# Optimization experiments

Measured on AMD Instinct MI355X. Metric: run time of the kernel, lower is better.

Reference implementation:

```python
import jax, jax.numpy as jnp
import numpy as np

DROPOUT_RATE = 0.1  # reference runs deterministically (dropout disabled), matching eval-mode math


def setup_inputs() -> dict:
    key = jax.random.key(0)
    k1, k2, k3 = jax.random.split(key, 3)
    BH, S, D = 32, 2048, 64   # batch*heads, seq_len, d_head
    B = 2                      # true batch (mask batch dim)
    q = jax.random.normal(k1, (BH, S, D), dtype=jnp.float32)
    k = jax.random.normal(k2, (BH, S, D), dtype=jnp.float32)
    v = jax.random.normal(k3, (BH, S, D), dtype=jnp.float32)
    mask = jnp.zeros((B, S, S), dtype=jnp.float32)  # additive mask
    return {"q": q, "k": k, "v": v, "mask": mask}


def reference(q, k, v, mask):
    # Scaled dot-product attention with additive mask.
    # q,k,v: [BH, S, D]; mask: [B, S, S], tiled along batch to BH.
    dk = jnp.asarray(k.shape[-1], dtype=jnp.float32)
    scores = jnp.einsum('bqd,bkd->bqk', q, k) / jnp.sqrt(dk)  # [BH, S, S]
    reps = q.shape[0] // mask.shape[0]
    mask_t = jnp.tile(mask, (reps, 1, 1))                     # [BH, S, S]
    attn = jax.nn.softmax(scores + mask_t, axis=-1)
    out = jnp.einsum('bqk,bkd->bqd', attn, v)                 # [BH, S, D]
    # K.dropout omitted: deterministic reference (eval mode / identity)
    return out
```

## Files before the change

kernel.cpp:

```cpp
#include <hip/hip_runtime.h>


constexpr int cBH = 32;
constexpr int cS  = 2048;
constexpr int cD  = 64;
constexpr int cQT = 128;
constexpr int cNT = cS / 64;

typedef __bf16 bf16x8 __attribute__((ext_vector_type(8)));
typedef __bf16 bf16x4 __attribute__((ext_vector_type(4)));
typedef float  f32x4  __attribute__((ext_vector_type(4)));

__device__ __forceinline__ unsigned short bfbits(float f) {
    return __builtin_bit_cast(unsigned short, (__bf16)f);
}
__device__ __forceinline__ bf16x4 pack4(f32x4 a) {
    bf16x4 r;
    r[0] = (__bf16)a[0]; r[1] = (__bf16)a[1];
    r[2] = (__bf16)a[2]; r[3] = (__bf16)a[3];
    return r;
}
__device__ __forceinline__ bf16x8 pack8s(f32x4 a, f32x4 b, float s) {
    bf16x8 r;
    r[0] = (__bf16)(a[0]*s); r[1] = (__bf16)(a[1]*s);
    r[2] = (__bf16)(a[2]*s); r[3] = (__bf16)(a[3]*s);
    r[4] = (__bf16)(b[0]*s); r[5] = (__bf16)(b[1]*s);
    r[6] = (__bf16)(b[2]*s); r[7] = (__bf16)(b[3]*s);
    return r;
}
__device__ __forceinline__ int fkey(int row) {
    return ((row & 7) ^ ((row >> 3) << 1)) & 7;
}
__device__ __forceinline__ int gkey(int d) {
    return (d ^ (d >> 3)) & 7;
}

__global__ __launch_bounds__(256, 2)
void sdpa_flash_kernel(const float* __restrict__ q,
                       const float* __restrict__ k,
                       const float* __restrict__ v,
                       const float* __restrict__ mask,
                       float* __restrict__ out)
{
    __shared__ unsigned short sK[2][64 * 64];
    __shared__ unsigned short sV[2][64 * 64];
    __shared__ unsigned short sP[4][32 * 64];

    const int tid  = threadIdx.x;
    const int wv   = tid >> 6;
    const int lane = tid & 63;
    const int quad = lane >> 4;
    const int ln   = lane & 15;

    const int fid = blockIdx.x;
    const int bh  = (fid & 7) | ((fid >> 7) << 3);
    const int qb  = ((fid >> 3) & 15) * cQT;
    const int mb  = bh & 1;

    const float L2E = 1.4426950408889634f;

    bf16x8 aq[2][2];
#pragma unroll
    for (int mg = 0; mg < 2; ++mg) {
        const float* qp = q + ((size_t)bh * cS + qb + wv * 32 + mg * 16 + ln) * cD + quad * 8;
        aq[mg][0] = pack8s(*(const f32x4*)(qp),      *(const f32x4*)(qp + 4),  0.125f * L2E);
        aq[mg][1] = pack8s(*(const f32x4*)(qp + 32), *(const f32x4*)(qp + 36), 0.125f * L2E);
    }

    f32x4 acc[2][4];
    float lsum[2][4];
#pragma unroll
    for (int mg = 0; mg < 2; ++mg)
#pragma unroll
        for (int t = 0; t < 4; ++t) {
            acc[mg][t] = (f32x4){0.f, 0.f, 0.f, 0.f};
            lsum[mg][t] = 0.f;
        }

    const int sr0 = tid >> 4;
    const int c4  = (tid & 15) << 2;
    const int ka0 = sr0 * 64 + (((c4 >> 3) ^ (sr0 & 7)) << 3) + (c4 & 7);
    const float* kg = k + (size_t)bh * cS * cD;
    const float* vg = v + (size_t)bh * cS * cD;

    const float* mq = mask + (size_t)mb * cS * cS
                           + (size_t)(qb + wv * 32 + quad * 4) * cS + ln;

#pragma unroll
    for (int j = 0; j < 4; ++j) {
        f32x4 kj = *(const f32x4*)(kg + j * 1024 + tid * 4);
        f32x4 vj = *(const f32x4*)(vg + j * 1024 + tid * 4);
        *(bf16x4*)&sK[0][ka0 + j * 1024] = pack4(kj);
#pragma unroll
        for (int i = 0; i < 4; ++i) {
            int d = c4 + i;
            sV[0][d * 64 + ((((j * 2) + (sr0 >> 3)) ^ gkey(d)) << 3) + (sr0 & 7)]
                = bfbits(vj[i]);
        }
    }
    float mc[2][4][4];
#pragma unroll
    for (int mg = 0; mg < 2; ++mg)
#pragma unroll
        for (int nt = 0; nt < 4; ++nt)
#pragma unroll
            for (int r = 0; r < 4; ++r)
                mc[mg][nt][r] = mq[(size_t)(mg * 16 + r) * cS + nt * 16];

    for (int kt = 0; kt < cNT; ++kt) {
        const int cur = kt & 1;
        const bool more = (kt + 1 < cNT);
        const int tnx = more ? kt + 1 : kt;

        f32x4 KP[4], VP[4];
        const int tb = tnx * 4096;
#pragma unroll
        for (int j = 0; j < 4; ++j) {
            KP[j] = *(const f32x4*)(kg + tb + j * 1024 + tid * 4);
            VP[j] = *(const f32x4*)(vg + tb + j * 1024 + tid * 4);
        }
        float mn[2][4][4];
#pragma unroll
        for (int mg = 0; mg < 2; ++mg)
#pragma unroll
            for (int nt = 0; nt < 4; ++nt)
#pragma unroll
                for (int r = 0; r < 4; ++r)
                    mn[mg][nt][r] = mq[(size_t)(mg * 16 + r) * cS + tnx * 64 + nt * 16];

        __syncthreads();

        const unsigned short* sKc = sK[cur];
        float p4[2][4][4];
#pragma unroll
        for (int nt = 0; nt < 4; ++nt) {
            bf16x8 b0 = *(const bf16x8*)(
                &sKc[(nt * 16 + ln) * 64 + ((quad ^ (ln & 7)) << 3)]);
            bf16x8 b1 = *(const bf16x8*)(
                &sKc[(nt * 16 + ln) * 64 + (((4 | quad) ^ (ln & 7)) << 3)]);
            f32x4 c0 = (f32x4){0.f, 0.f, 0.f, 0.f};
            f32x4 c1 = (f32x4){0.f, 0.f, 0.f, 0.f};
            c0 = __builtin_amdgcn_mfma_f32_16x16x32_bf16(aq[0][0], b0, c0, 0, 0, 0);
            c1 = __builtin_amdgcn_mfma_f32_16x16x32_bf16(aq[1][0], b0, c1, 0, 0, 0);
            c0 = __builtin_amdgcn_mfma_f32_16x16x32_bf16(aq[0][1], b1, c0, 0, 0, 0);
            c1 = __builtin_amdgcn_mfma_f32_16x16x32_bf16(aq[1][1], b1, c1, 0, 0, 0);
#pragma unroll
            for (int r = 0; r < 4; ++r) {
                p4[0][nt][r] = __builtin_amdgcn_exp2f(fmaf(mc[0][nt][r], L2E, c0[r]));
                p4[1][nt][r] = __builtin_amdgcn_exp2f(fmaf(mc[1][nt][r], L2E, c1[r]));
            }
        }
#pragma unroll
        for (int mg = 0; mg < 2; ++mg)
#pragma unroll
            for (int r = 0; r < 4; ++r)
                lsum[mg][r] += (p4[mg][0][r] + p4[mg][1][r])
                             + (p4[mg][2][r] + p4[mg][3][r]);

#pragma unroll
        for (int mg = 0; mg < 2; ++mg)
#pragma unroll
            for (int nt = 0; nt < 4; ++nt)
#pragma unroll
                for (int r = 0; r < 4; ++r) {
                    int row = mg * 16 + quad * 4 + r;
                    int blk = ((nt * 2 + (ln >> 3)) ^ fkey(row)) << 3;
                    sP[wv][row * 64 + blk + (ln & 7)] = bfbits(p4[mg][nt][r]);
                }

        const unsigned short* sVc = sV[cur];
#pragma unroll
        for (int ks = 0; ks < 2; ++ks) {
            bf16x8 ap0 = *(const bf16x8*)(
                &sP[wv][ln * 64 + ((((ks << 2) | quad) ^ fkey(ln)) << 3)]);
            bf16x8 ap1 = *(const bf16x8*)(
                &sP[wv][(16 + ln) * 64 + ((((ks << 2) | quad) ^ fkey(16 + ln)) << 3)]);
#pragma unroll
            for (int dt = 0; dt < 4; ++dt) {
                int d = dt * 16 + ln;
                bf16x8 bv = *(const bf16x8*)(
                    &sVc[d * 64 + ((((ks << 2) | quad) ^ gkey(d)) << 3)]);
                acc[0][dt] = __builtin_amdgcn_mfma_f32_16x16x32_bf16(ap0, bv, acc[0][dt], 0, 0, 0);
                acc[1][dt] = __builtin_amdgcn_mfma_f32_16x16x32_bf16(ap1, bv, acc[1][dt], 0, 0, 0);
            }
        }

        if (more) {
            unsigned short* sKn = sK[cur ^ 1];
            unsigned short* sVn = sV[cur ^ 1];
#pragma unroll
            for (int j = 0; j < 4; ++j) {
                *(bf16x4*)&sKn[ka0 + j * 1024] = pack4(KP[j]);
#pragma unroll
                for (int i = 0; i < 4; ++i) {
                    int d = c4 + i;
                    sVn[d * 64 + ((((j * 2) + (sr0 >> 3)) ^ gkey(d)) << 3) + (sr0 & 7)]
                        = bfbits(VP[j][i]);
                }
            }
        }
#pragma unroll
        for (int mg = 0; mg < 2; ++mg)
#pragma unroll
            for (int nt = 0; nt < 4; ++nt)
#pragma unroll
                for (int r = 0; r < 4; ++r)
                    mc[mg][nt][r] = mn[mg][nt][r];
    }

#pragma unroll
    for (int off = 1; off < 16; off <<= 1)
#pragma unroll
        for (int mg = 0; mg < 2; ++mg)
#pragma unroll
            for (int r = 0; r < 4; ++r)
                lsum[mg][r] += __shfl_xor(lsum[mg][r], off, 64);
#pragma unroll
    for (int mg = 0; mg < 2; ++mg) {
        float rl[4];
#pragma unroll
        for (int r = 0; r < 4; ++r) rl[r] = 1.0f / lsum[mg][r];
#pragma unroll
        for (int dt = 0; dt < 4; ++dt)
#pragma unroll
            for (int r = 0; r < 4; ++r)
                out[((size_t)bh * cS + qb + wv * 32 + mg * 16 + quad * 4 + r) * cD
                    + dt * 16 + ln] = acc[mg][dt][r] * rl[r];
    }
}

extern "C" void kernel_launch(void* const* d_in, const int* in_sizes, int n_in,
                              void* d_out, int out_size, void* d_ws, size_t ws_size,
                              hipStream_t stream) {
    const float* q = (const float*)d_in[0];
    const float* k = (const float*)d_in[1];
    const float* v = (const float*)d_in[2];
    const float* m = (const float*)d_in[3];
    float* o = (float*)d_out;
    sdpa_flash_kernel<<<dim3(512), 256, 0, stream>>>(q, k, v, m, o);
}
```

Before: 178.7 us.

## Process two key tiles per iteration with single-buffered shared memory staging

The kernel now handles 128 keys per loop iteration, as two 64-key tiles held in the two shared buffers, instead of one double-buffered 64-key tile. Mask values are loaded for the current pair rather than prefetched one step ahead. A second barrier is added before the next pair is written into shared memory. The aim is to halve loop and barrier overhead per key and expose more independent MFMA work. In exchange it doubles prefetch registers, removes compute/store overlap because writes now wait behind a barrier, and grows the sP buffer, which may hurt occupancy at two blocks per CU.

```diff
diff --git a/kernel.cpp b/kernel.cpp
--- a/kernel.cpp
+++ b/kernel.cpp
@@ -5,7 +5,7 @@
 constexpr int cS  = 2048;
 constexpr int cD  = 64;
 constexpr int cQT = 128;
-constexpr int cNT = cS / 64;
+constexpr int cNP = cS / 128;
 
 typedef __bf16 bf16x8 __attribute__((ext_vector_type(8)));
 typedef __bf16 bf16x4 __attribute__((ext_vector_type(4)));
@@ -44,7 +44,7 @@
 {
     __shared__ unsigned short sK[2][64 * 64];
     __shared__ unsigned short sV[2][64 * 64];
-    __shared__ unsigned short sP[4][32 * 64];
+    __shared__ unsigned short sP[4][2][32 * 64];
 
     const int tid  = threadIdx.x;
     const int wv   = tid >> 6;
@@ -82,80 +82,84 @@
     const int ka0 = sr0 * 64 + (((c4 >> 3) ^ (sr0 & 7)) << 3) + (c4 & 7);
     const float* kg = k + (size_t)bh * cS * cD;
     const float* vg = v + (size_t)bh * cS * cD;
-
     const float* mq = mask + (size_t)mb * cS * cS
                            + (size_t)(qb + wv * 32 + quad * 4) * cS + ln;
 
 #pragma unroll
-    for (int j = 0; j < 4; ++j) {
-        f32x4 kj = *(const f32x4*)(kg + j * 1024 + tid * 4);
-        f32x4 vj = *(const f32x4*)(vg + j * 1024 + tid * 4);
-        *(bf16x4*)&sK[0][ka0 + j * 1024] = pack4(kj);
-#pragma unroll
-        for (int i = 0; i < 4; ++i) {
-            int d = c4 + i;
-            sV[0][d * 64 + ((((j * 2) + (sr0 >> 3)) ^ gkey(d)) << 3) + (sr0 & 7)]
-                = bfbits(vj[i]);
-        }
-    }
-    float mc[2][4][4];
-#pragma unroll
-    for (int mg = 0; mg < 2; ++mg)
-#pragma unroll
-        for (int nt = 0; nt < 4; ++nt)
+    for (int t = 0; t < 2; ++t)
+#pragma unroll
+        for (int j = 0; j < 4; ++j) {
+            f32x4 kj = *(const f32x4*)(kg + t * 4096 + j * 1024 + tid * 4);
+            f32x4 vj = *(const f32x4*)(vg + t * 4096 + j * 1024 + tid * 4);
+            *(bf16x4*)&sK[t][ka0 + j * 1024] = pack4(kj);
+#pragma unroll
+            for (int i = 0; i < 4; ++i) {
+                int d = c4 + i;
+                sV[t][d * 64 + ((((j * 2) + (sr0 >> 3)) ^ gkey(d)) << 3) + (sr0 & 7)]
+                    = bfbits(vj[i]);
+            }
+        }
+
+    for (int pt = 0; pt < cNP; ++pt) {
+        const int base = pt * 2;
+        const bool more = (pt + 1 < cNP);
+        const int nb = more ? base + 2 : base;
+
+        f32x4 KPe[4], VPe[4], KPo[4], VPo[4];
+#pragma unroll
+        for (int j = 0; j < 4; ++j) {
+            KPe[j] = *(const f32x4*)(kg + (size_t)nb * 4096 + j * 1024 + tid * 4);
+            VPe[j] = *(const f32x4*)(vg + (size_t)nb * 4096 + j * 1024 + tid * 4);
+            KPo[j] = *(const f32x4*)(kg + (size_t)(nb + 1) * 4096 + j * 1024 + tid * 4);
+            VPo[j] = *(const f32x4*)(vg + (size_t)(nb + 1) * 4096 + j * 1024 + tid * 4);
+        }
+        float mcE[2][4][4], mcO[2][4][4];
+#pragma unroll
+        for (int mg = 0; mg < 2; ++mg)
+#pragma unroll
+            for (int nt = 0; nt < 4; ++nt)
+#pragma unroll
+                for (int r = 0; r < 4; ++r) {
+                    const float* mrow = mq + (size_t)(mg * 16 + r) * cS + base * 64 + nt * 16;
+                    mcE[mg][nt][r] = mrow[0];
+                    mcO[mg][nt][r] = mrow[64];
+                }
+
+        __syncthreads();
+
+        float pE[2][4][4], pO[2][4][4];
+#pragma unroll
+        for (int nt = 0; nt < 4; ++nt) {
+            const int rb = (nt * 16 + ln) * 64;
+            const int x0 = (quad ^ (ln & 7)) << 3;
+            const int x1 = ((4 | quad) ^ (ln & 7)) << 3;
+            bf16x8 be0 = *(const bf16x8*)(&sK[0][rb + x0]);
+            bf16x8 be1 = *(const bf16x8*)(&sK[0][rb + x1]);
+            bf16x8 bo0 = *(const bf16x8*)(&sK[1][rb + x0]);
+            bf16x8 bo1 = *(const bf16x8*)(&sK[1][rb + x1]);
+            f32x4 ce0 = (f32x4){0.f,0.f,0.f,0.f}, ce1 = ce0, co0 = ce0, co1 = ce0;
+            ce0 = __builtin_amdgcn_mfma_f32_16x16x32_bf16(aq[0][0], be0, ce0, 0, 0, 0);
+            ce1 = __builtin_amdgcn_mfma_f32_16x16x32_bf16(aq[1][0], be0, ce1, 0, 0, 0);
+            co0 = __builtin_amdgcn_mfma_f32_16x16x32_bf16(aq[0][0], bo0, co0, 0, 0, 0);
+            co1 = __builtin_amdgcn_mfma_f32_16x16x32_bf16(aq[1][0], bo0, co1, 0, 0, 0);
+            ce0 = __builtin_amdgcn_mfma_f32_16x16x32_bf16(aq[0][1], be1, ce0, 0, 0, 0);
+            ce1 = __builtin_amdgcn_mfma_f32_16x16x32_bf16(aq[1][1], be1, ce1, 0, 0, 0);
+            co0 = __builtin_amdgcn_mfma_f32_16x16x32_bf16(aq[0][1], bo1, co0, 0, 0, 0);
+            co1 = __builtin_amdgcn_mfma_f32_16x16x32_bf16(aq[1][1], bo1, co1, 0, 0, 0);
+#pragma unroll
+            for (int r = 0; r < 4; ++r) {
+                pE[0][nt][r] = __builtin_amdgcn_exp2f(fmaf(mcE[0][nt][r], L2E, ce0[r]));
+                pE[1][nt][r] = __builtin_amdgcn_exp2f(fmaf(mcE[1][nt][r], L2E, ce1[r]));
+                pO[0][nt][r] = __builtin_amdgcn_exp2f(fmaf(mcO[0][nt][r], L2E, co0[r]));
+                pO[1][nt][r] = __builtin_amdgcn_exp2f(fmaf(mcO[1][nt][r], L2E, co1[r]));
+            }
+        }
+#pragma unroll
+        for (int mg = 0; mg < 2; ++mg)
 #pragma unroll
             for (int r = 0; r < 4; ++r)
-                mc[mg][nt][r] = mq[(size_t)(mg * 16 + r) * cS + nt * 16];
-
-    for (int kt = 0; kt < cNT; ++kt) {
-        const int cur = kt & 1;
-        const bool more = (kt + 1 < cNT);
-        const int tnx = more ? kt + 1 : kt;
-
-        f32x4 KP[4], VP[4];
-        const int tb = tnx * 4096;
-#pragma unroll
-        for (int j = 0; j < 4; ++j) {
-            KP[j] = *(const f32x4*)(kg + tb + j * 1024 + tid * 4);
-            VP[j] = *(const f32x4*)(vg + tb + j * 1024 + tid * 4);
-        }
-        float mn[2][4][4];
-#pragma unroll
-        for (int mg = 0; mg < 2; ++mg)
-#pragma unroll
-            for (int nt = 0; nt < 4; ++nt)
-#pragma unroll
-                for (int r = 0; r < 4; ++r)
-                    mn[mg][nt][r] = mq[(size_t)(mg * 16 + r) * cS + tnx * 64 + nt * 16];
-
-        __syncthreads();
-
-        const unsigned short* sKc = sK[cur];
-        float p4[2][4][4];
-#pragma unroll
-        for (int nt = 0; nt < 4; ++nt) {
-            bf16x8 b0 = *(const bf16x8*)(
-                &sKc[(nt * 16 + ln) * 64 + ((quad ^ (ln & 7)) << 3)]);
-            bf16x8 b1 = *(const bf16x8*)(
-                &sKc[(nt * 16 + ln) * 64 + (((4 | quad) ^ (ln & 7)) << 3)]);
-            f32x4 c0 = (f32x4){0.f, 0.f, 0.f, 0.f};
-            f32x4 c1 = (f32x4){0.f, 0.f, 0.f, 0.f};
-            c0 = __builtin_amdgcn_mfma_f32_16x16x32_bf16(aq[0][0], b0, c0, 0, 0, 0);
-            c1 = __builtin_amdgcn_mfma_f32_16x16x32_bf16(aq[1][0], b0, c1, 0, 0, 0);
-            c0 = __builtin_amdgcn_mfma_f32_16x16x32_bf16(aq[0][1], b1, c0, 0, 0, 0);
-            c1 = __builtin_amdgcn_mfma_f32_16x16x32_bf16(aq[1][1], b1, c1, 0, 0, 0);
-#pragma unroll
-            for (int r = 0; r < 4; ++r) {
-                p4[0][nt][r] = __builtin_amdgcn_exp2f(fmaf(mc[0][nt][r], L2E, c0[r]));
-                p4[1][nt][r] = __builtin_amdgcn_exp2f(fmaf(mc[1][nt][r], L2E, c1[r]));
-            }
-        }
-#pragma unroll
-        for (int mg = 0; mg < 2; ++mg)
-#pragma unroll
-            for (int r = 0; r < 4; ++r)
-                lsum[mg][r] += (p4[mg][0][r] + p4[mg][1][r])
-                             + (p4[mg][2][r] + p4[mg][3][r]);
+                lsum[mg][r] += (pE[mg][0][r] + pE[mg][1][r]) + (pE[mg][2][r] + pE[mg][3][r])
+                             + (pO[mg][0][r] + pO[mg][1][r]) + (pO[mg][2][r] + pO[mg][3][r]);
 
 #pragma unroll
         for (int mg = 0; mg < 2; ++mg)
@@ -165,47 +169,47 @@
                 for (int r = 0; r < 4; ++r) {
                     int row = mg * 16 + quad * 4 + r;
                     int blk = ((nt * 2 + (ln >> 3)) ^ fkey(row)) << 3;
-                    sP[wv][row * 64 + blk + (ln & 7)] = bfbits(p4[mg][nt][r]);
-                }
-
-        const unsigned short* sVc = sV[cur];
-#pragma unroll
-        for (int ks = 0; ks < 2; ++ks) {
-            bf16x8 ap0 = *(const bf16x8*)(
-                &sP[wv][ln * 64 + ((((ks << 2) | quad) ^ fkey(ln)) << 3)]);
-            bf16x8 ap1 = *(const bf16x8*)(
-                &sP[wv][(16 + ln) * 64 + ((((ks << 2) | quad) ^ fkey(16 + ln)) << 3)]);
-#pragma unroll
-            for (int dt = 0; dt < 4; ++dt) {
-                int d = dt * 16 + ln;
-                bf16x8 bv = *(const bf16x8*)(
-                    &sVc[d * 64 + ((((ks << 2) | quad) ^ gkey(d)) << 3)]);
-                acc[0][dt] = __builtin_amdgcn_mfma_f32_16x16x32_bf16(ap0, bv, acc[0][dt], 0, 0, 0);
-                acc[1][dt] = __builtin_amdgcn_mfma_f32_16x16x32_bf16(ap1, bv, acc[1][dt], 0, 0, 0);
-            }
-        }
+                    sP[wv][0][row * 64 + blk + (ln & 7)] = bfbits(pE[mg][nt][r]);
+                    sP[wv][1][row * 64 + blk + (ln & 7)] = bfbits(pO[mg][nt][r]);
+                }
+
+#pragma unroll
+        for (int t = 0; t < 2; ++t) {
+            const unsigned short* sPt = &sP[wv][t][0];
+            const unsigned short* sVt = sV[t];
+#pragma unroll
+            for (int ks = 0; ks < 2; ++ks) {
+                bf16x8 ap0 = *(const bf16x8*)(
+                    &sPt[ln * 64 + ((((ks << 2) | quad) ^ fkey(ln)) << 3)]);
+                bf16x8 ap1 = *(const bf16x8*)(
+                    &sPt[(16 + ln) * 64 + ((((ks << 2) | quad) ^ fkey(16 + ln)) << 3)]);
+#pragma unroll
+                for (int dt = 0; dt < 4; ++dt) {
+                    int d = dt * 16 + ln;
+                    bf16x8 bv = *(const bf16x8*)(
+                        &sVt[d * 64 + ((((ks << 2) | quad) ^ gkey(d)) << 3)]);
+                    acc[0][dt] = __builtin_amdgcn_mfma_f32_16x16x32_bf16(ap0, bv, acc[0][dt], 0, 0, 0);
+                    acc[1][dt] = __builtin_amdgcn_mfma_f32_16x16x32_bf16(ap1, bv, acc[1][dt], 0, 0, 0);
+                }
+            }
+        }
+
+        __syncthreads();
 
         if (more) {
-            unsigned short* sKn = sK[cur ^ 1];
-            unsigned short* sVn = sV[cur ^ 1];
 #pragma unroll
             for (int j = 0; j < 4; ++j) {
-                *(bf16x4*)&sKn[ka0 + j * 1024] = pack4(KP[j]);
+                *(bf16x4*)&sK[0][ka0 + j * 1024] = pack4(KPe[j]);
+                *(bf16x4*)&sK[1][ka0 + j * 1024] = pack4(KPo[j]);
 #pragma unroll
                 for (int i = 0; i < 4; ++i) {
                     int d = c4 + i;
-                    sVn[d * 64 + ((((j * 2) + (sr0 >> 3)) ^ gkey(d)) << 3) + (sr0 & 7)]
-                        = bfbits(VP[j][i]);
-                }
-            }
-        }
-#pragma unroll
-        for (int mg = 0; mg < 2; ++mg)
-#pragma unroll
-            for (int nt = 0; nt < 4; ++nt)
-#pragma unroll
-                for (int r = 0; r < 4; ++r)
-                    mc[mg][nt][r] = mn[mg][nt][r];
+                    int va = d * 64 + ((((j * 2) + (sr0 >> 3)) ^ gkey(d)) << 3) + (sr0 & 7);
+                    sV[0][va] = bfbits(VPe[j][i]);
+                    sV[1][va] = bfbits(VPo[j][i]);
+                }
+            }
+        }
     }
 
 #pragma unroll
```

After: 175.4 us. Within noise of the previous version (-1.8%).

## Compute transposed S tile and feed P to PV MFMA via ds_bpermute instead of LDS

Applied to the files above, without the earlier changes.

Swaps the MFMA operands in the QK^T product so each lane holds a query row's scores across keys. The softmax probabilities are then redistributed into the PV A-operand layout with ds_bpermute rather than a round trip through a per-wave shared-memory P buffer. This removes the sP LDS stores, loads and buffer, and simplifies the row-sum reduction to two shuffles at the end. Mask loads become vectorized f32x4 row reads fetched in the current iteration instead of being prefetched one tile ahead, which may expose mask load latency.

```diff
diff --git a/kernel.cpp b/kernel.cpp
--- a/kernel.cpp
+++ b/kernel.cpp
@@ -27,9 +27,6 @@
     r[4] = (__bf16)(b[0]*s); r[5] = (__bf16)(b[1]*s);
     r[6] = (__bf16)(b[2]*s); r[7] = (__bf16)(b[3]*s);
     return r;
-}
-__device__ __forceinline__ int fkey(int row) {
-    return ((row & 7) ^ ((row >> 3) << 1)) & 7;
 }
 __device__ __forceinline__ int gkey(int d) {
     return (d ^ (d >> 3)) & 7;
@@ -44,7 +41,6 @@
 {
     __shared__ unsigned short sK[2][64 * 64];
     __shared__ unsigned short sV[2][64 * 64];
-    __shared__ unsigned short sP[4][32 * 64];
 
     const int tid  = threadIdx.x;
     const int wv   = tid >> 6;
@@ -68,14 +64,12 @@
     }
 
     f32x4 acc[2][4];
-    float lsum[2][4];
+    float lsum[2] = {0.f, 0.f};
 #pragma unroll
     for (int mg = 0; mg < 2; ++mg)
 #pragma unroll
-        for (int t = 0; t < 4; ++t) {
+        for (int t = 0; t < 4; ++t)
             acc[mg][t] = (f32x4){0.f, 0.f, 0.f, 0.f};
-            lsum[mg][t] = 0.f;
-        }
 
     const int sr0 = tid >> 4;
     const int c4  = (tid & 15) << 2;
@@ -83,8 +77,13 @@
     const float* kg = k + (size_t)bh * cS * cD;
     const float* vg = v + (size_t)bh * cS * cD;
 
-    const float* mq = mask + (size_t)mb * cS * cS
-                           + (size_t)(qb + wv * 32 + quad * 4) * cS + ln;
+    const float* mrow0 = mask + (size_t)mb * cS * cS
+                              + (size_t)(qb + wv * 32 + ln) * cS + quad * 4;
+    const float* mrow1 = mrow0 + (size_t)16 * cS;
+
+    const int permA = ((((lane >> 4) & 1) << 5) + ln) << 2;
+    const int permB = permA + 64;
+    const int shft  = (lane & 32) >> 1;
 
 #pragma unroll
     for (int j = 0; j < 4; ++j) {
@@ -98,20 +97,18 @@
                 = bfbits(vj[i]);
         }
     }
-    float mc[2][4][4];
-#pragma unroll
-    for (int mg = 0; mg < 2; ++mg)
-#pragma unroll
-        for (int nt = 0; nt < 4; ++nt)
-#pragma unroll
-            for (int r = 0; r < 4; ++r)
-                mc[mg][nt][r] = mq[(size_t)(mg * 16 + r) * cS + nt * 16];
 
     for (int kt = 0; kt < cNT; ++kt) {
         const int cur = kt & 1;
         const bool more = (kt + 1 < cNT);
         const int tnx = more ? kt + 1 : kt;
 
+        f32x4 mk[2][4];
+#pragma unroll
+        for (int nt = 0; nt < 4; ++nt) {
+            mk[0][nt] = *(const f32x4*)(mrow0 + kt * 64 + nt * 16);
+            mk[1][nt] = *(const f32x4*)(mrow1 + kt * 64 + nt * 16);
+        }
         f32x4 KP[4], VP[4];
         const int tb = tnx * 4096;
 #pragma unroll
@@ -119,14 +116,6 @@
             KP[j] = *(const f32x4*)(kg + tb + j * 1024 + tid * 4);
             VP[j] = *(const f32x4*)(vg + tb + j * 1024 + tid * 4);
         }
-        float mn[2][4][4];
-#pragma unroll
-        for (int mg = 0; mg < 2; ++mg)
-#pragma unroll
-            for (int nt = 0; nt < 4; ++nt)
-#pragma unroll
-                for (int r = 0; r < 4; ++r)
-                    mn[mg][nt][r] = mq[(size_t)(mg * 16 + r) * cS + tnx * 64 + nt * 16];
 
         __syncthreads();
 
@@ -134,56 +123,56 @@
         float p4[2][4][4];
 #pragma unroll
         for (int nt = 0; nt < 4; ++nt) {
-            bf16x8 b0 = *(const bf16x8*)(
+            bf16x8 kf0 = *(const bf16x8*)(
                 &sKc[(nt * 16 + ln) * 64 + ((quad ^ (ln & 7)) << 3)]);
-            bf16x8 b1 = *(const bf16x8*)(
+            bf16x8 kf1 = *(const bf16x8*)(
                 &sKc[(nt * 16 + ln) * 64 + (((4 | quad) ^ (ln & 7)) << 3)]);
             f32x4 c0 = (f32x4){0.f, 0.f, 0.f, 0.f};
             f32x4 c1 = (f32x4){0.f, 0.f, 0.f, 0.f};
-            c0 = __builtin_amdgcn_mfma_f32_16x16x32_bf16(aq[0][0], b0, c0, 0, 0, 0);
-            c1 = __builtin_amdgcn_mfma_f32_16x16x32_bf16(aq[1][0], b0, c1, 0, 0, 0);
-            c0 = __builtin_amdgcn_mfma_f32_16x16x32_bf16(aq[0][1], b1, c0, 0, 0, 0);
-            c1 = __builtin_amdgcn_mfma_f32_16x16x32_bf16(aq[1][1], b1, c1, 0, 0, 0);
+            c0 = __builtin_amdgcn_mfma_f32_16x16x32_bf16(kf0, aq[0][0], c0, 0, 0, 0);
+            c1 = __builtin_amdgcn_mfma_f32_16x16x32_bf16(kf0, aq[1][0], c1, 0, 0, 0);
+            c0 = __builtin_amdgcn_mfma_f32_16x16x32_bf16(kf1, aq[0][1], c0, 0, 0, 0);
+            c1 = __builtin_amdgcn_mfma_f32_16x16x32_bf16(kf1, aq[1][1], c1, 0, 0, 0);
 #pragma unroll
             for (int r = 0; r < 4; ++r) {
-                p4[0][nt][r] = __builtin_amdgcn_exp2f(fmaf(mc[0][nt][r], L2E, c0[r]));
-                p4[1][nt][r] = __builtin_amdgcn_exp2f(fmaf(mc[1][nt][r], L2E, c1[r]));
+                p4[0][nt][r] = __builtin_amdgcn_exp2f(fmaf(mk[0][nt][r], L2E, c0[r]));
+                p4[1][nt][r] = __builtin_amdgcn_exp2f(fmaf(mk[1][nt][r], L2E, c1[r]));
             }
         }
 #pragma unroll
         for (int mg = 0; mg < 2; ++mg)
 #pragma unroll
-            for (int r = 0; r < 4; ++r)
-                lsum[mg][r] += (p4[mg][0][r] + p4[mg][1][r])
-                             + (p4[mg][2][r] + p4[mg][3][r]);
-
+            for (int nt = 0; nt < 4; ++nt)
+                lsum[mg] += ((p4[mg][nt][0] + p4[mg][nt][1])
+                           + (p4[mg][nt][2] + p4[mg][nt][3]));
+
+        const unsigned short* sVc = sV[cur];
 #pragma unroll
         for (int mg = 0; mg < 2; ++mg)
 #pragma unroll
-            for (int nt = 0; nt < 4; ++nt)
+            for (int ks = 0; ks < 2; ++ks) {
+                int rA[4], rB[4];
 #pragma unroll
                 for (int r = 0; r < 4; ++r) {
-                    int row = mg * 16 + quad * 4 + r;
-                    int blk = ((nt * 2 + (ln >> 3)) ^ fkey(row)) << 3;
-                    sP[wv][row * 64 + blk + (ln & 7)] = bfbits(p4[mg][nt][r]);
-                }
-
-        const unsigned short* sVc = sV[cur];
-#pragma unroll
-        for (int ks = 0; ks < 2; ++ks) {
-            bf16x8 ap0 = *(const bf16x8*)(
-                &sP[wv][ln * 64 + ((((ks << 2) | quad) ^ fkey(ln)) << 3)]);
-            bf16x8 ap1 = *(const bf16x8*)(
-                &sP[wv][(16 + ln) * 64 + ((((ks << 2) | quad) ^ fkey(16 + ln)) << 3)]);
-#pragma unroll
-            for (int dt = 0; dt < 4; ++dt) {
-                int d = dt * 16 + ln;
-                bf16x8 bv = *(const bf16x8*)(
-                    &sVc[d * 64 + ((((ks << 2) | quad) ^ gkey(d)) << 3)]);
-                acc[0][dt] = __builtin_amdgcn_mfma_f32_16x16x32_bf16(ap0, bv, acc[0][dt], 0, 0, 0);
-                acc[1][dt] = __builtin_amdgcn_mfma_f32_16x16x32_bf16(ap1, bv, acc[1][dt], 0, 0, 0);
+                    int packed = (int)bfbits(p4[mg][2 * ks][r])
+                               | ((int)bfbits(p4[mg][2 * ks + 1][r]) << 16);
+                    rA[r] = __builtin_amdgcn_ds_bpermute(permA, packed);
+                    rB[r] = __builtin_amdgcn_ds_bpermute(permB, packed);
+                }
+                bf16x8 ap;
+#pragma unroll
+                for (int r = 0; r < 4; ++r) {
+                    ap[r]     = __builtin_bit_cast(__bf16, (unsigned short)(rA[r] >> shft));
+                    ap[4 + r] = __builtin_bit_cast(__bf16, (unsigned short)(rB[r] >> shft));
+                }
+#pragma unroll
+                for (int dt = 0; dt < 4; ++dt) {
+                    int d = dt * 16 + ln;
+                    bf16x8 bv = *(const bf16x8*)(
+                        &sVc[d * 64 + ((((ks << 2) | quad) ^ gkey(d)) << 3)]);
+                    acc[mg][dt] = __builtin_amdgcn_mfma_f32_16x16x32_bf16(ap, bv, acc[mg][dt], 0, 0, 0);
+                }
             }
-        }
 
         if (more) {
             unsigned short* sKn = sK[cur ^ 1];
@@ -199,27 +188,18 @@
                 }
             }
         }
-#pragma unroll
-        for (int mg = 0; mg < 2; ++mg)
-#pragma unroll
-            for (int nt = 0; nt < 4; ++nt)
-#pragma unroll
-                for (int r = 0; r < 4; ++r)
-                    mc[mg][nt][r] = mn[mg][nt][r];
-    }
-
-#pragma unroll
-    for (int off = 1; off < 16; off <<= 1)
-#pragma unroll
-        for (int mg = 0; mg < 2; ++mg)
-#pragma unroll
-            for (int r = 0; r < 4; ++r)
-                lsum[mg][r] += __shfl_xor(lsum[mg][r], off, 64);
+    }
+
 #pragma unroll
     for (int mg = 0; mg < 2; ++mg) {
+        float s = lsum[mg];
+        s += __shfl_xor(s, 16, 64);
+        s += __shfl_xor(s, 32, 64);
+        float rs = 1.0f / s;
         float rl[4];
 #pragma unroll
-        for (int r = 0; r < 4; ++r) rl[r] = 1.0f / lsum[mg][r];
+        for (int r = 0; r < 4; ++r)
+            rl[r] = __shfl(rs, quad * 4 + r, 64);
 #pragma unroll
         for (int dt = 0; dt < 4; ++dt)
 #pragma unroll
```

Result: slower. 183.4 us (+2.6%).
